# Kernel tuning notes

Measured on AMD Instinct MI355X. Metric: run time of the kernel, lower is better.

## Reference

```python
import jax, jax.numpy as jnp
import numpy as np

B, N = 512, 256

def setup_inputs() -> dict:
    key = jax.random.key(0)
    k1, k2 = jax.random.split(key)
    D1 = jax.random.normal(k1, (B, N, N), dtype=jnp.float32)
    D2 = jax.random.normal(k2, (B, N, N), dtype=jnp.float32)
    types1 = jnp.zeros((B, N), dtype=jnp.int32)
    types2 = jnp.zeros((B, N), dtype=jnp.int32)
    return {"D1": D1, "D2": D2, "types1": types1, "types2": types2}


def reference(D1, D2, types1, types2):
    # Hungarian cost: cost[b, i, j] = |mean_k D1[b, k, i] - mean_k D2[b, k, j]|.
    # For an absolute-difference cost between two scalar profiles, the optimal
    # linear assignment (what scipy's linear_sum_assignment returns inside the
    # original tf.py_function) matches sorted values to sorted values; with a
    # point-type constraint, it matches sorted values within each type group.
    # We therefore compute the exact optimal permutation via a lexicographic
    # sort on (type, mean-distance) for each side, which is fully vectorized
    # and avoids the host-side CPU loop of the original layer.
    a = jnp.mean(D1, axis=1)  # [B, N] column means of D1
    b = jnp.mean(D2, axis=1)  # [B, N]

    def optimal_perm(a_row, b_row, t1, t2):
        # sort primarily by type, secondarily by value (lexsort: last key primary)
        order1 = jnp.lexsort((a_row, t1))  # [N] atom indices of D1 in sorted order
        order2 = jnp.lexsort((b_row, t2))  # [N] target positions in sorted order
        # atom order1[k] is placed at position order2[k]
        return jnp.zeros_like(order1).at[order2].set(order1)  # perm[j] = source atom for slot j

    perm = jax.vmap(optimal_perm)(a, b, types1, types2)  # [B, N]

    # Symmetric reorder of rows and columns of D1 by perm.
    D1_rows = jnp.take_along_axis(D1, perm[:, :, None], axis=1)          # [B, N, N]
    D1_reordered = jnp.take_along_axis(D1_rows, perm[:, None, :], axis=2)  # [B, N, N]
    types1_reordered = jnp.take_along_axis(types1, perm, axis=1)         # [B, N]

    # The original layer applies tf.stop_gradient to both outputs.
    D1_reordered = jax.lax.stop_gradient(D1_reordered)
    types1_reordered = jax.lax.stop_gradient(types1_reordered)
    return D1_reordered, types1_reordered
```

## Files before the change

### kernel.cpp

```cpp
#include <hip/hip_runtime.h>
#include <hip/hip_bf16.h>

#define BATCH 512
#define NN 256

__global__ __launch_bounds__(256) void col_means_kernel(
    const float* __restrict__ D1, const float* __restrict__ D2,
    float* __restrict__ am, float* __restrict__ bm) {
  const int b = blockIdx.x;
  const float* __restrict__ src = blockIdx.y ? D2 : D1;
  float* __restrict__ dst = blockIdx.y ? bm : am;
  const int c = threadIdx.x;

  const float* base = src + (size_t)b * (NN * NN) + c;

  float half_sum[2];
#pragma unroll
  for (int h = 0; h < 2; ++h) {
    const float* hbase = base + (size_t)(h * 128) * NN;
    float r[8];
#pragma unroll
    for (int t = 0; t < 8; ++t) r[t] = hbase[(size_t)t * NN];
    for (int m = 1; m < 16; ++m) {
#pragma unroll
      for (int t = 0; t < 8; ++t) r[t] += hbase[(size_t)(8 * m + t) * NN];
    }
    const float s01 = r[0] + r[1];
    const float s23 = r[2] + r[3];
    const float s45 = r[4] + r[5];
    const float s67 = r[6] + r[7];
    half_sum[h] = (s01 + s23) + (s45 + s67);
  }
  const float tot = half_sum[0] + half_sum[1];
  dst[(size_t)b * NN + c] = tot * (1.0f / 256.0f);
}

__global__ __launch_bounds__(256) void rank_perm_kernel(
    const float* __restrict__ am, const float* __restrict__ bm,
    const int* __restrict__ t1, const int* __restrict__ t2,
    int* __restrict__ perm, float* __restrict__ types_out) {
  const int b = blockIdx.x;
  const int tid = threadIdx.x;

  __shared__ float va[NN];
  __shared__ int ta[NN];
  __shared__ int ord1[NN];
  __shared__ int ord2[NN];
  __shared__ int plds[NN];

  va[tid] = am[b * NN + tid];
  ta[tid] = t1[b * NN + tid];
  __syncthreads();
  {
    const float vi = va[tid];
    const int ti = ta[tid];
    int r = 0;
#pragma unroll 4
    for (int j = 0; j < NN; ++j) {
      const int tj = ta[j];
      const float vj = va[j];
      const bool less =
          (tj < ti) || (tj == ti && (vj < vi || (vj == vi && j < tid)));
      r += less ? 1 : 0;
    }
    ord1[r] = tid;
  }
  __syncthreads();

  va[tid] = bm[b * NN + tid];
  ta[tid] = t2[b * NN + tid];
  __syncthreads();
  {
    const float vi = va[tid];
    const int ti = ta[tid];
    int r = 0;
#pragma unroll 4
    for (int j = 0; j < NN; ++j) {
      const int tj = ta[j];
      const float vj = va[j];
      const bool less =
          (tj < ti) || (tj == ti && (vj < vi || (vj == vi && j < tid)));
      r += less ? 1 : 0;
    }
    ord2[r] = tid;
  }
  __syncthreads();

  plds[ord2[tid]] = ord1[tid];
  __syncthreads();

  perm[b * NN + tid] = plds[tid];
  types_out[b * NN + tid] = (float)t1[b * NN + plds[tid]];
}

__global__ __launch_bounds__(256) void reorder_kernel(
    const float* __restrict__ D1, const int* __restrict__ perm,
    float* __restrict__ out) {
  const int b = blockIdx.x >> 6;
  const int ig = blockIdx.x & 63;
  const int tid = threadIdx.x;
  const int lane = tid & 63;
  const int w = tid >> 6;

  __shared__ int plds[NN];
  __shared__ float4 rows[4][64];

  plds[tid] = perm[b * NN + tid];
  __syncthreads();

  const int i = ig * 4 + w;
  const int pi = plds[i];
  const float* rsrc = D1 + ((size_t)b * NN + pi) * NN;
  rows[w][lane] = *(const float4*)(rsrc + 4 * lane);
  __syncthreads();

  const float* rf = (const float*)&rows[w][0];
  const int j0 = 4 * lane;
  float4 o;
  o.x = rf[plds[j0 + 0]];
  o.y = rf[plds[j0 + 1]];
  o.z = rf[plds[j0 + 2]];
  o.w = rf[plds[j0 + 3]];
  *(float4*)(out + ((size_t)b * NN + i) * NN + j0) = o;
}

extern "C" void kernel_launch(void* const* d_in, const int* in_sizes, int n_in,
                              void* d_out, int out_size, void* d_ws, size_t ws_size,
                              hipStream_t stream) {
  const float* D1 = (const float*)d_in[0];
  const float* D2 = (const float*)d_in[1];
  const int* t1 = (const int*)d_in[2];
  const int* t2 = (const int*)d_in[3];

  float* out = (float*)d_out;
  float* types_out = out + (size_t)BATCH * NN * NN;

  float* am = (float*)d_ws;
  float* bm = am + (size_t)BATCH * NN;
  int* perm = (int*)(bm + (size_t)BATCH * NN);

  col_means_kernel<<<dim3(BATCH, 2), 256, 0, stream>>>(D1, D2, am, bm);
  rank_perm_kernel<<<BATCH, 256, 0, stream>>>(am, bm, t1, t2, perm, types_out);
  reorder_kernel<<<BATCH * 64, 256, 0, stream>>>(D1, perm, out);
}
```

Measured before the change: 368.3 us.

## Fuse column means, ranking and symmetric reorder into one per-batch kernel

Replaces the three-kernel pipeline with a single kernel where each 512-thread block handles one batch: it computes both column-mean vectors with float4 loads, ranks both sides concurrently, builds the permutation in shared memory, then streams the reordered rows with a one-row-ahead prefetch. This removes two launches, the workspace round trips for means and permutation, and lets the D1 re-read likely hit cache. In exchange, only 512 blocks do all the streaming, which may limit memory-level parallelism, and the reorder phase is serialized over 32 iterations per warp.

```diff
diff --git a/kernel.cpp b/kernel.cpp
--- a/kernel.cpp
+++ b/kernel.cpp
@@ -4,124 +4,117 @@
 #define BATCH 512
 #define NN 256
 
-__global__ __launch_bounds__(256) void col_means_kernel(
-    const float* __restrict__ D1, const float* __restrict__ D2,
-    float* __restrict__ am, float* __restrict__ bm) {
-  const int b = blockIdx.x;
-  const float* __restrict__ src = blockIdx.y ? D2 : D1;
-  float* __restrict__ dst = blockIdx.y ? bm : am;
-  const int c = threadIdx.x;
-
-  const float* base = src + (size_t)b * (NN * NN) + c;
-
-  float half_sum[2];
-#pragma unroll
-  for (int h = 0; h < 2; ++h) {
-    const float* hbase = base + (size_t)(h * 128) * NN;
-    float r[8];
-#pragma unroll
-    for (int t = 0; t < 8; ++t) r[t] = hbase[(size_t)t * NN];
-    for (int m = 1; m < 16; ++m) {
-#pragma unroll
-      for (int t = 0; t < 8; ++t) r[t] += hbase[(size_t)(8 * m + t) * NN];
-    }
-    const float s01 = r[0] + r[1];
-    const float s23 = r[2] + r[3];
-    const float s45 = r[4] + r[5];
-    const float s67 = r[6] + r[7];
-    half_sum[h] = (s01 + s23) + (s45 + s67);
-  }
-  const float tot = half_sum[0] + half_sum[1];
-  dst[(size_t)b * NN + c] = tot * (1.0f / 256.0f);
+__device__ __forceinline__ float4 f4add(float4 x, float4 y) {
+  return make_float4(x.x + y.x, x.y + y.y, x.z + y.z, x.w + y.w);
 }
 
-__global__ __launch_bounds__(256) void rank_perm_kernel(
-    const float* __restrict__ am, const float* __restrict__ bm,
+__global__ __launch_bounds__(512, 4) void fused_hungarian_kernel(
+    const float* __restrict__ D1, const float* __restrict__ D2,
     const int* __restrict__ t1, const int* __restrict__ t2,
-    int* __restrict__ perm, float* __restrict__ types_out) {
+    float* __restrict__ out, float* __restrict__ types_out) {
   const int b = blockIdx.x;
   const int tid = threadIdx.x;
 
-  __shared__ float va[NN];
-  __shared__ int ta[NN];
-  __shared__ int ord1[NN];
-  __shared__ int ord2[NN];
-  __shared__ int plds[NN];
+  __shared__ float4 partial4[2][4][64];
+  __shared__ float va[NN], vb[NN];
+  __shared__ int ta[NN], tb[NN];
+  __shared__ int ord1[NN], ord2[NN], plds[NN];
+  __shared__ float4 rows[8][64];
 
-  va[tid] = am[b * NN + tid];
-  ta[tid] = t1[b * NN + tid];
+  {
+    const int c4 = tid & 63;
+    const int slot = tid >> 6;
+    const int mat = slot >> 2;
+    const int s2 = slot & 3;
+    const int h = s2 >> 1;
+    const int tq = s2 & 1;
+    const float* __restrict__ src = (mat ? D2 : D1) + (size_t)b * (NN * NN);
+    const float* cb = src + (size_t)(h * 128 + 4 * tq) * NN + 4 * c4;
+
+    float4 r0 = *(const float4*)(cb + (size_t)0 * NN);
+    float4 r1 = *(const float4*)(cb + (size_t)1 * NN);
+    float4 r2 = *(const float4*)(cb + (size_t)2 * NN);
+    float4 r3 = *(const float4*)(cb + (size_t)3 * NN);
+#pragma unroll
+    for (int m = 1; m < 16; ++m) {
+      const float* p = cb + (size_t)(8 * m) * NN;
+      r0 = f4add(r0, *(const float4*)(p + (size_t)0 * NN));
+      r1 = f4add(r1, *(const float4*)(p + (size_t)1 * NN));
+      r2 = f4add(r2, *(const float4*)(p + (size_t)2 * NN));
+      r3 = f4add(r3, *(const float4*)(p + (size_t)3 * NN));
+    }
+    partial4[mat][s2][c4] = f4add(f4add(r0, r1), f4add(r2, r3));
+  }
+  if (tid < NN) ta[tid] = t1[b * NN + tid];
+  else          tb[tid - NN] = t2[b * NN + (tid - NN)];
   __syncthreads();
+
   {
-    const float vi = va[tid];
-    const int ti = ta[tid];
+    const int mat = tid >> 8;
+    const int c = tid & 255;
+    const float p0 = ((const float*)partial4[mat][0])[c];
+    const float p1 = ((const float*)partial4[mat][1])[c];
+    const float p2 = ((const float*)partial4[mat][2])[c];
+    const float p3 = ((const float*)partial4[mat][3])[c];
+    const float tot = (p0 + p1) + (p2 + p3);
+    const float mean = tot * (1.0f / 256.0f);
+    if (mat == 0) va[c] = mean; else vb[c] = mean;
+  }
+  __syncthreads();
+
+  {
+    const int side = tid >> 8;
+    const int c = tid & 255;
+    const float* __restrict__ vv = side ? vb : va;
+    const int* __restrict__ tt = side ? tb : ta;
+    const float vi = vv[c];
+    const int ti = tt[c];
     int r = 0;
 #pragma unroll 4
     for (int j = 0; j < NN; ++j) {
-      const int tj = ta[j];
-      const float vj = va[j];
+      const int tj = tt[j];
+      const float vj = vv[j];
       const bool less =
-          (tj < ti) || (tj == ti && (vj < vi || (vj == vi && j < tid)));
+          (tj < ti) || (tj == ti && (vj < vi || (vj == vi && j < c)));
       r += less ? 1 : 0;
     }
-    ord1[r] = tid;
+    if (side == 0) ord1[r] = c;
+    else           ord2[r] = c;
   }
   __syncthreads();
+  if (tid < NN) plds[ord2[tid]] = ord1[tid];
+  __syncthreads();
+  if (tid < NN) types_out[b * NN + tid] = (float)ta[plds[tid]];
 
-  va[tid] = bm[b * NN + tid];
-  ta[tid] = t2[b * NN + tid];
-  __syncthreads();
   {
-    const float vi = va[tid];
-    const int ti = ta[tid];
-    int r = 0;
-#pragma unroll 4
-    for (int j = 0; j < NN; ++j) {
-      const int tj = ta[j];
-      const float vj = va[j];
-      const bool less =
-          (tj < ti) || (tj == ti && (vj < vi || (vj == vi && j < tid)));
-      r += less ? 1 : 0;
+    const int w = tid >> 6;
+    const int lane = tid & 63;
+    const int j0 = 4 * lane;
+    const int pj0 = plds[j0 + 0];
+    const int pj1 = plds[j0 + 1];
+    const int pj2 = plds[j0 + 2];
+    const int pj3 = plds[j0 + 3];
+    const float* __restrict__ Db = D1 + (size_t)b * (NN * NN);
+    float* __restrict__ outb = out + (size_t)b * (NN * NN);
+    const float* rowf = (const float*)&rows[w][0];
+
+    int pi = plds[w];
+    float4 vst = *(const float4*)(Db + (size_t)pi * NN + j0);
+    for (int iter = 0; iter < 32; ++iter) {
+      const int i = iter * 8 + w;
+      rows[w][lane] = vst;
+      if (iter < 31) {
+        const int pin = plds[(iter + 1) * 8 + w];
+        vst = *(const float4*)(Db + (size_t)pin * NN + j0);
+      }
+      float4 o;
+      o.x = rowf[pj0];
+      o.y = rowf[pj1];
+      o.z = rowf[pj2];
+      o.w = rowf[pj3];
+      *(float4*)(outb + (size_t)i * NN + j0) = o;
     }
-    ord2[r] = tid;
   }
-  __syncthreads();
-
-  plds[ord2[tid]] = ord1[tid];
-  __syncthreads();
-
-  perm[b * NN + tid] = plds[tid];
-  types_out[b * NN + tid] = (float)t1[b * NN + plds[tid]];
-}
-
-__global__ __launch_bounds__(256) void reorder_kernel(
-    const float* __restrict__ D1, const int* __restrict__ perm,
-    float* __restrict__ out) {
-  const int b = blockIdx.x >> 6;
-  const int ig = blockIdx.x & 63;
-  const int tid = threadIdx.x;
-  const int lane = tid & 63;
-  const int w = tid >> 6;
-
-  __shared__ int plds[NN];
-  __shared__ float4 rows[4][64];
-
-  plds[tid] = perm[b * NN + tid];
-  __syncthreads();
-
-  const int i = ig * 4 + w;
-  const int pi = plds[i];
-  const float* rsrc = D1 + ((size_t)b * NN + pi) * NN;
-  rows[w][lane] = *(const float4*)(rsrc + 4 * lane);
-  __syncthreads();
-
-  const float* rf = (const float*)&rows[w][0];
-  const int j0 = 4 * lane;
-  float4 o;
-  o.x = rf[plds[j0 + 0]];
-  o.y = rf[plds[j0 + 1]];
-  o.z = rf[plds[j0 + 2]];
-  o.w = rf[plds[j0 + 3]];
-  *(float4*)(out + ((size_t)b * NN + i) * NN + j0) = o;
 }
 
 extern "C" void kernel_launch(void* const* d_in, const int* in_sizes, int n_in,
@@ -135,11 +128,6 @@
   float* out = (float*)d_out;
   float* types_out = out + (size_t)BATCH * NN * NN;
 
-  float* am = (float*)d_ws;
-  float* bm = am + (size_t)BATCH * NN;
-  int* perm = (int*)(bm + (size_t)BATCH * NN);
-
-  col_means_kernel<<<dim3(BATCH, 2), 256, 0, stream>>>(D1, D2, am, bm);
-  rank_perm_kernel<<<BATCH, 256, 0, stream>>>(am, bm, t1, t2, perm, types_out);
-  reorder_kernel<<<BATCH * 64, 256, 0, stream>>>(D1, perm, out);
+  fused_hungarian_kernel<<<BATCH, 512, 0, stream>>>(D1, D2, t1, t2, out,
+                                                    types_out);
 }
```

Result: faster. 346.0 us (-6.1%).
